# Performance work log

Hardware: AMD Instinct MI355X
Metric: run time of the kernel (lower is better)

## Reference

```python
import jax, jax.numpy as jnp
import numpy as np

N_NODES = 50000
N_EDGES = 1600000
N_FEAT = 128
EMB = 128
N_CLASSES = 10
N_GRAPHS = 512


def setup_inputs() -> dict:
    key = jax.random.key(0)
    ks = jax.random.split(key, 12)
    x = jax.random.normal(ks[0], (N_NODES, N_FEAT), dtype=jnp.float32)
    edge_index = jax.random.randint(ks[1], (2, N_EDGES), 0, N_NODES, dtype=jnp.int64)
    batch = jnp.sort(jax.random.randint(ks[2], (N_NODES,), 0, N_GRAPHS, dtype=jnp.int64))
    def glorot(k, fan_in, fan_out):
        lim = jnp.sqrt(6.0 / (fan_in + fan_out)).astype(jnp.float32)
        return jax.random.uniform(k, (fan_in, fan_out), jnp.float32, -lim, lim)
    W0 = glorot(ks[3], N_FEAT, EMB); b0 = jnp.zeros((EMB,), jnp.float32)
    W1 = glorot(ks[4], EMB, EMB);    b1 = jnp.zeros((EMB,), jnp.float32)
    W2 = glorot(ks[5], EMB, EMB);    b2 = jnp.zeros((EMB,), jnp.float32)
    Wout = glorot(ks[6], EMB, N_CLASSES)
    bout = jnp.zeros((N_CLASSES,), jnp.float32)
    return {"x": x, "edge_index": edge_index, "batch": batch,
            "W0": W0, "b0": b0, "W1": W1, "b1": b1, "W2": W2, "b2": b2,
            "Wout": Wout, "bout": bout}


def _gcn_conv(x, W, b, src, dst, norm, n_nodes):
    # PyG GCNConv: h = x @ W; aggregate norm * h[src] into dst; add bias.
    h = x @ W                                  # [N, out]
    msg = h[src] * norm[:, None]               # [E+N, out] gather (incl. self-loops)
    out = jax.ops.segment_sum(msg, dst, num_segments=n_nodes)
    return out + b


def reference(x, edge_index, batch, W0, b0, W1, b1, W2, b2, Wout, bout):
    n_nodes = x.shape[0]
    # add self-loops (GCNConv default add_self_loops=True)
    loops = jnp.arange(n_nodes, dtype=edge_index.dtype)
    src = jnp.concatenate([edge_index[0], loops])
    dst = jnp.concatenate([edge_index[1], loops])
    # symmetric normalization D^{-1/2} (A+I) D^{-1/2}
    deg = jax.ops.segment_sum(jnp.ones_like(dst, dtype=x.dtype), dst,
                              num_segments=n_nodes)
    deg_inv_sqrt = jnp.where(deg > 0, jax.lax.rsqrt(jnp.maximum(deg, 1.0)), 0.0)
    norm = deg_inv_sqrt[src] * deg_inv_sqrt[dst]   # [E+N]
    out = jnp.tanh(_gcn_conv(x, W0, b0, src, dst, norm, n_nodes))
    out = jnp.tanh(_gcn_conv(out, W1, b1, src, dst, norm, n_nodes))
    out = _gcn_conv(out, W2, b2, src, dst, norm, n_nodes)
    # global mean pool over per-node graph ids
    sums = jax.ops.segment_sum(out, batch, num_segments=N_GRAPHS)
    counts = jax.ops.segment_sum(jnp.ones((n_nodes,), out.dtype), batch,
                                 num_segments=N_GRAPHS)
    pooled = sums / jnp.maximum(counts, 1.0)[:, None]   # [G, EMB]
    logits = pooled @ Wout + bout                        # [G, C]
    return jax.nn.log_softmax(logits, axis=1)
```

## Files before the change

### kernel.cpp

```cpp
#include <hip/hip_runtime.h>
#include <math.h>


#define BLK_EDGES 4096
#define MAXB 128
#define ECAP 2048
#define WS_STRIDE 136

typedef __attribute__((ext_vector_type(8))) short bf16x8;
typedef __attribute__((ext_vector_type(4))) float f32x4;

static __device__ inline unsigned short f2bf(float f) {
    unsigned u = __float_as_uint(f);
    unsigned r = (u + 0x7FFFu + ((u >> 16) & 1u)) >> 16;
    return (unsigned short)r;
}
static __device__ inline float bf_lo(unsigned u) { return __uint_as_float(u << 16); }
static __device__ inline float bf_hi(unsigned u) { return __uint_as_float(u & 0xFFFF0000u); }
static __device__ inline unsigned char f2fp8(float v) {
    v = fminf(fmaxf(v, -240.f), 240.f);
    int u = __builtin_amdgcn_cvt_pk_fp8_f32(v, v, 0, false);
    return (unsigned char)(u & 0xFF);
}

__global__ __launch_bounds__(256) void blk_hist(const int* __restrict__ dst,
        int* __restrict__ histT, int E, int NBLK, int NB) {
    __shared__ int h[MAXB];
    int blk = blockIdx.x, t = threadIdx.x;
    for (int i = t; i < NB; i += 256) h[i] = 0;
    __syncthreads();
    int lo = blk * BLK_EDGES;
    int hi = min(E, lo + BLK_EDGES);
    for (int i = lo + t; i < hi; i += 256)
        atomicAdd(&h[dst[i] >> 9], 1);
    __syncthreads();
    for (int i = t; i < NB; i += 256) histT[i * NBLK + blk] = h[i];
}

__global__ void scan_block(const int* __restrict__ cnt, int* __restrict__ off,
                           int* __restrict__ bsum, int n) {
    __shared__ int lds[256];
    int t = threadIdx.x;
    int i = blockIdx.x * 256 + t;
    int v = (i < n) ? cnt[i] : 0;
    lds[t] = v;
    __syncthreads();
    for (int d = 1; d < 256; d <<= 1) {
        int add = (t >= d) ? lds[t - d] : 0;
        __syncthreads();
        lds[t] += add;
        __syncthreads();
    }
    if (i < n) off[i] = lds[t] - v;
    if (t == 255) bsum[blockIdx.x] = lds[255];
}

__global__ void scan_top(const int* __restrict__ bsum, int* __restrict__ boff,
                         int nblocks) {
    __shared__ int lds[256];
    int t = threadIdx.x;
    int v = (t < nblocks) ? bsum[t] : 0;
    lds[t] = v;
    __syncthreads();
    for (int d = 1; d < 256; d <<= 1) {
        int add = (t >= d) ? lds[t - d] : 0;
        __syncthreads();
        lds[t] += add;
        __syncthreads();
    }
    if (t < nblocks) boff[t] = lds[t] - v;
}

__global__ __launch_bounds__(256) void scatter_packed(const int* __restrict__ src,
        const int* __restrict__ dst, const int* __restrict__ P,
        const int* __restrict__ boff, unsigned* __restrict__ packed,
        int E, int NBLK, int NB) {
    __shared__ int cur[MAXB];
    int blk = blockIdx.x, t = threadIdx.x;
    for (int i = t; i < NB; i += 256) {
        int idx = i * NBLK + blk;
        cur[i] = P[idx] + boff[idx >> 8];
    }
    __syncthreads();
    int lo = blk * BLK_EDGES;
    int hi = min(E, lo + BLK_EDGES);
    for (int i = lo + t; i < hi; i += 256) {
        int d = dst[i];
        int pos = atomicAdd(&cur[d >> 9], 1);
        packed[pos] = ((unsigned)d << 16) | (unsigned)src[i];
    }
}

__global__ __launch_bounds__(256) void bucket_build(const unsigned* __restrict__ packed,
        const int* __restrict__ P, const int* __restrict__ boff, int* __restrict__ off,
        float* __restrict__ dis, unsigned short* __restrict__ csr16,
        int E, int NBLK, int N, int NB) {
    __shared__ int cnt[512];
    __shared__ int loc[512];
    __shared__ int ps[256];
    int b = blockIdx.x, t = threadIdx.x;
    int i0 = b * NBLK, i1 = (b + 1) * NBLK;
    int start = P[i0] + boff[i0 >> 8];
    int end   = (b == NB - 1) ? E : (P[i1] + boff[i1 >> 8]);
    cnt[t] = 0; cnt[t + 256] = 0;
    __syncthreads();
    for (int i = start + t; i < end; i += 256)
        atomicAdd(&cnt[(packed[i] >> 16) & 511], 1);
    __syncthreads();
    int c0 = cnt[2 * t], c1 = cnt[2 * t + 1];
    ps[t] = c0 + c1;
    __syncthreads();
    for (int d = 1; d < 256; d <<= 1) {
        int add = (t >= d) ? ps[t - d] : 0;
        __syncthreads();
        ps[t] += add;
        __syncthreads();
    }
    int pexcl = ps[t] - (c0 + c1);
    loc[2 * t]     = start + pexcl;
    loc[2 * t + 1] = start + pexcl + c0;
    __syncthreads();
    int node0 = b * 512;
    for (int l = t; l < 512; l += 256) {
        int node = node0 + l;
        if (node < N) {
            off[node] = loc[l];
            dis[node] = rsqrtf((float)cnt[l] + 1.0f);
        }
    }
    if (b == NB - 1 && t == 0) off[N] = E;
    __syncthreads();
    for (int i = start + t; i < end; i += 256) {
        unsigned p = packed[i];
        int l = (p >> 16) & 511;
        int pos = atomicAdd(&loc[l], 1);
        csr16[pos] = (unsigned short)(p & 0xFFFFu);
    }
}

__global__ __launch_bounds__(256) void prep(const float* __restrict__ W0,
        const float* __restrict__ W1, const float* __restrict__ W2,
        unsigned short* __restrict__ wt0, unsigned short* __restrict__ wt1,
        unsigned short* __restrict__ wt2, const float* __restrict__ x,
        unsigned short* __restrict__ xb, int n4) {
    int i = blockIdx.x * 256 + threadIdx.x;
    if (i < 3 * 16384) {
        int w = i >> 14, j = i & 16383;
        int k = j >> 7, n2 = j & 127;
        const float* Wp = (w == 0) ? W0 : (w == 1) ? W1 : W2;
        unsigned short* Wt = (w == 0) ? wt0 : (w == 1) ? wt1 : wt2;
        Wt[n2 * 128 + k] = f2bf(Wp[k * 128 + n2]);
    } else {
        int j = i - 3 * 16384;
        if (j < n4) {
            float4 f = ((const float4*)x)[j];
            ushort4 o = {f2bf(f.x), f2bf(f.y), f2bf(f.z), f2bf(f.w)};
            ((ushort4*)xb)[j] = o;
        }
    }
}

__global__ __launch_bounds__(128) void gemm_mfma(const unsigned short* __restrict__ A16,
        const unsigned short* __restrict__ Wt, const float* __restrict__ dis,
        unsigned char* __restrict__ Hs8, int n) {
    __shared__ unsigned short Ws[128 * WS_STRIDE];
    int t = threadIdx.x;
    for (int i = t; i < 128 * 16; i += 128) {
        int r = i >> 4, j = i & 15;
        uint4 u = ((const uint4*)(Wt + r * 128))[j];
        *(uint4*)&Ws[r * WS_STRIDE + j * 8] = u;
    }
    __syncthreads();

    int wave = t >> 6, lane = t & 63;
    int quad = lane >> 4, l16 = lane & 15;
    int row0 = blockIdx.x * 64 + wave * 32;

    int ra0 = row0 + l16;      if (ra0 >= n) ra0 = n - 1;
    int ra1 = row0 + 16 + l16; if (ra1 >= n) ra1 = n - 1;

    f32x4 acc[2][8];
    const f32x4 z = {0.f, 0.f, 0.f, 0.f};
#pragma unroll
    for (int mi = 0; mi < 2; ++mi)
#pragma unroll
        for (int ni = 0; ni < 8; ++ni) acc[mi][ni] = z;

#pragma unroll
    for (int ks = 0; ks < 4; ++ks) {
        int kof = ks * 32 + quad * 8;
        bf16x8 a0 = *(const bf16x8*)(A16 + (size_t)ra0 * 128 + kof);
        bf16x8 a1 = *(const bf16x8*)(A16 + (size_t)ra1 * 128 + kof);
        bf16x8 b[8];
#pragma unroll
        for (int ni = 0; ni < 8; ++ni)
            b[ni] = *(const bf16x8*)&Ws[(ni * 16 + l16) * WS_STRIDE + kof];
#pragma unroll
        for (int ni = 0; ni < 8; ++ni) {
            acc[0][ni] = __builtin_amdgcn_mfma_f32_16x16x32_bf16(a0, b[ni], acc[0][ni], 0, 0, 0);
            acc[1][ni] = __builtin_amdgcn_mfma_f32_16x16x32_bf16(a1, b[ni], acc[1][ni], 0, 0, 0);
        }
    }
#pragma unroll
    for (int mi = 0; mi < 2; ++mi) {
        int rb = row0 + mi * 16 + quad * 4;
#pragma unroll
        for (int reg = 0; reg < 4; ++reg) {
            int r = rb + reg;
            if (r < n) {
                float dv = dis[r];
#pragma unroll
                for (int ni = 0; ni < 8; ++ni)
                    Hs8[(size_t)r * 128 + ni * 16 + l16] = f2fp8(acc[mi][ni][reg] * dv);
            }
        }
    }
}

template<int DO_TANH, int OUT_BF16>
__global__ __launch_bounds__(256) void aggregate3(const unsigned char* __restrict__ hs,
    const unsigned short* __restrict__ csr, const int* __restrict__ off,
    const float* __restrict__ dis, const float* __restrict__ bias,
    void* __restrict__ outp, int n) {
    __shared__ unsigned short eidx[ECAP];
    int t = threadIdx.x;
    int node0 = blockIdx.x * 4;
    int b0 = off[node0];
    int top = node0 + 4 < n ? node0 + 4 : n;
    int b4 = off[top];
    int mblk = b4 - b0;
    bool staged = (mblk <= ECAP);
    if (staged)
        for (int i = t; i < mblk; i += 256) eidx[i] = csr[b0 + i];
    __syncthreads();

    int node = node0 + (t >> 6);
    if (node >= n) return;
    int lane = t & 63;
    int half = lane >> 5;
    int fq = lane & 31;
    const unsigned* H = (const unsigned*)hs;

    int e0 = off[node];
    int e1 = off[node + 1];
    int le0 = e0 - b0;
    int m = e1 - e0;
    float ax = 0.f, ay = 0.f, az = 0.f, aw = 0.f;

    unsigned va[8], vb[8];
    auto sumB = [&](unsigned* v) {
#pragma unroll
        for (int j = 0; j < 8; ++j) {
            ax += __builtin_amdgcn_cvt_f32_fp8(v[j], 0);
            ay += __builtin_amdgcn_cvt_f32_fp8(v[j], 1);
            az += __builtin_amdgcn_cvt_f32_fp8(v[j], 2);
            aw += __builtin_amdgcn_cvt_f32_fp8(v[j], 3);
        }
    };
    auto loadL = [&](int i, unsigned* v) {
        int s[8];
#pragma unroll
        for (int j = 0; j < 8; ++j) s[j] = eidx[le0 + i + half + 2 * j];
#pragma unroll
        for (int j = 0; j < 8; ++j) v[j] = H[(size_t)s[j] * 32 + fq];
    };
    auto loadG = [&](int i, unsigned* v) {
        int s[8];
#pragma unroll
        for (int j = 0; j < 8; ++j) s[j] = csr[e0 + i + half + 2 * j];
#pragma unroll
        for (int j = 0; j < 8; ++j) v[j] = H[(size_t)s[j] * 32 + fq];
    };

    int nfull = m & ~15;
    if (staged) {
        if (nfull) {
            int B = nfull >> 4;
            loadL(0, va);
            int k = 1;
            for (; k + 1 < B; k += 2) {
                loadL(k << 4, vb);       sumB(va);
                loadL((k + 1) << 4, va); sumB(vb);
            }
            if (k < B) { loadL(k << 4, vb); sumB(va); sumB(vb); }
            else       { sumB(va); }
        }
        for (int e = nfull + half; e < m; e += 2) {
            unsigned v = H[(size_t)eidx[le0 + e] * 32 + fq];
            ax += __builtin_amdgcn_cvt_f32_fp8(v, 0);
            ay += __builtin_amdgcn_cvt_f32_fp8(v, 1);
            az += __builtin_amdgcn_cvt_f32_fp8(v, 2);
            aw += __builtin_amdgcn_cvt_f32_fp8(v, 3);
        }
    } else {
        if (nfull) {
            int B = nfull >> 4;
            loadG(0, va);
            int k = 1;
            for (; k + 1 < B; k += 2) {
                loadG(k << 4, vb);       sumB(va);
                loadG((k + 1) << 4, va); sumB(vb);
            }
            if (k < B) { loadG(k << 4, vb); sumB(va); sumB(vb); }
            else       { sumB(va); }
        }
        for (int e = nfull + half; e < m; e += 2) {
            unsigned v = H[(size_t)csr[e0 + e] * 32 + fq];
            ax += __builtin_amdgcn_cvt_f32_fp8(v, 0);
            ay += __builtin_amdgcn_cvt_f32_fp8(v, 1);
            az += __builtin_amdgcn_cvt_f32_fp8(v, 2);
            aw += __builtin_amdgcn_cvt_f32_fp8(v, 3);
        }
    }

    ax += __shfl_xor(ax, 32, 64);
    ay += __shfl_xor(ay, 32, 64);
    az += __shfl_xor(az, 32, 64);
    aw += __shfl_xor(aw, 32, 64);

    unsigned sv = H[(size_t)node * 32 + fq];
    ax += __builtin_amdgcn_cvt_f32_fp8(sv, 0);
    ay += __builtin_amdgcn_cvt_f32_fp8(sv, 1);
    az += __builtin_amdgcn_cvt_f32_fp8(sv, 2);
    aw += __builtin_amdgcn_cvt_f32_fp8(sv, 3);

    float dn = dis[node];
    float4 bv = ((const float4*)bias)[fq];
    float ox = fmaf(dn, ax, bv.x);
    float oy = fmaf(dn, ay, bv.y);
    float oz = fmaf(dn, az, bv.z);
    float ow = fmaf(dn, aw, bv.w);
    if (DO_TANH) {
        ox = tanhf(ox); oy = tanhf(oy); oz = tanhf(oz); ow = tanhf(ow);
    }
    if (half == 0) {
        if (OUT_BF16) {
            uint2 o;
            o.x = (unsigned)f2bf(ox) | ((unsigned)f2bf(oy) << 16);
            o.y = (unsigned)f2bf(oz) | ((unsigned)f2bf(ow) << 16);
            ((uint2*)outp)[(size_t)node * 32 + fq] = o;
        } else {
            float4 o = {ox, oy, oz, ow};
            *(float4*)((float*)outp + (size_t)node * 128 + fq * 4) = o;
        }
    }
}

__global__ __launch_bounds__(256) void pool_head(const float* __restrict__ act,
    const int* __restrict__ batch, const float* __restrict__ Wout,
    const float* __restrict__ bout, float* __restrict__ out, int n, int C) {
    __shared__ float psum[4][128];
    __shared__ float l[16];
    __shared__ float stats[2];
    int g = blockIdx.x;
    int t = threadIdx.x;
    int w = t >> 6;
    int lane = t & 63;
    int lo = 0, hi = n;
    while (lo < hi) { int mid = (lo + hi) >> 1; if (batch[mid] < g) lo = mid + 1; else hi = mid; }
    int lo1 = lo, hi1 = n;
    while (lo1 < hi1) { int mid = (lo1 + hi1) >> 1; if (batch[mid] < g + 1) lo1 = mid + 1; else hi1 = mid; }
    float ax = 0.f, ay = 0.f;
    for (int i = lo + w; i < lo1; i += 4) {
        const float2 v = *(const float2*)(act + (size_t)i * 128 + lane * 2);
        ax += v.x;
        ay += v.y;
    }
    psum[w][2 * lane]     = ax;
    psum[w][2 * lane + 1] = ay;
    __syncthreads();
    if (w == 0) {
        int cnt = lo1 - lo;
        float inv = 1.0f / (float)(cnt > 0 ? cnt : 1);
        float sx = (psum[0][2 * lane] + psum[1][2 * lane])
                 + (psum[2][2 * lane] + psum[3][2 * lane]);
        float sy = (psum[0][2 * lane + 1] + psum[1][2 * lane + 1])
                 + (psum[2][2 * lane + 1] + psum[3][2 * lane + 1]);
        psum[0][2 * lane]     = sx * inv;
        psum[0][2 * lane + 1] = sy * inv;
    }
    __syncthreads();
    if (t < C) {
        float acc = bout[t];
        for (int f = 0; f < 128; ++f)
            acc = fmaf(psum[0][f], Wout[(size_t)f * C + t], acc);
        l[t] = acc;
    }
    __syncthreads();
    if (t == 0) {
        float m = -1e30f;
        for (int c = 0; c < C; ++c) m = fmaxf(m, l[c]);
        float s = 0.f;
        for (int c = 0; c < C; ++c) s += expf(l[c] - m);
        stats[0] = m;
        stats[1] = logf(s);
    }
    __syncthreads();
    if (t < C) out[(size_t)g * C + t] = l[t] - stats[0] - stats[1];
}

extern "C" void kernel_launch(void* const* d_in, const int* in_sizes, int n_in,
                              void* d_out, int out_size, void* d_ws, size_t ws_size,
                              hipStream_t stream) {
    const float* x     = (const float*)d_in[0];
    const int*   edge  = (const int*)d_in[1];
    const int*   batch = (const int*)d_in[2];
    const float* W0 = (const float*)d_in[3];
    const float* b0 = (const float*)d_in[4];
    const float* W1 = (const float*)d_in[5];
    const float* b1 = (const float*)d_in[6];
    const float* W2 = (const float*)d_in[7];
    const float* b2 = (const float*)d_in[8];
    const float* Wout = (const float*)d_in[9];
    const float* bout = (const float*)d_in[10];
    float* out = (float*)d_out;

    const int N = in_sizes[0] / 128;
    const int E = in_sizes[1] / 2;
    const int C = in_sizes[10];
    const int G = out_size / C;

    const int* src = edge;
    const int* dst = edge + E;

    const int NBLK = (E + BLK_EDGES - 1) / BLK_EDGES;
    const int NB   = (N + 511) / 512;
    const int NBQ  = NB * NBLK;

    char* p = (char*)d_ws;
    auto alloc = [&](size_t bytes) -> void* {
        void* r = (void*)p;
        p += (bytes + 255) & ~(size_t)255;
        return r;
    };
    unsigned char* hs = (unsigned char*)alloc((size_t)N * 128);
    float* act    = (float*)alloc((size_t)N * 128 * 4);
    float* dis    = (float*)alloc((size_t)N * 4);
    int*   off    = (int*)alloc((size_t)(N + 1) * 4);
    int*   P      = (int*)alloc((size_t)(NBQ + 1) * 4);
    int*   bsum   = (int*)alloc(256 * 4);
    int*   boff   = (int*)alloc(256 * 4);
    unsigned* packed = (unsigned*)alloc((size_t)E * 4);
    unsigned short* csr16 = (unsigned short*)alloc((size_t)E * 2);
    unsigned short* wt0 = (unsigned short*)alloc(128 * 128 * 2);
    unsigned short* wt1 = (unsigned short*)alloc(128 * 128 * 2);
    unsigned short* wt2 = (unsigned short*)alloc(128 * 128 * 2);

    const int sb = (NBQ + 255) / 256;

    blk_hist<<<NBLK, 256, 0, stream>>>(dst, P, E, NBLK, NB);
    scan_block<<<sb, 256, 0, stream>>>(P, P, bsum, NBQ);
    scan_top<<<1, 256, 0, stream>>>(bsum, boff, sb);
    scatter_packed<<<NBLK, 256, 0, stream>>>(src, dst, P, boff, packed, E, NBLK, NB);
    bucket_build<<<NB, 256, 0, stream>>>(packed, P, boff, off, dis, csr16, E, NBLK, N, NB);

    unsigned short* actb = (unsigned short*)act;
    const int n4 = N * 32;
    prep<<<(3 * 16384 + n4 + 255) / 256, 256, 0, stream>>>(W0, W1, W2, wt0, wt1, wt2,
                                                           x, actb, n4);

    const int gb = (N + 63) / 64;
    const int ab = (N + 3) / 4;

    gemm_mfma<<<gb, 128, 0, stream>>>(actb, wt0, dis, hs, N);
    aggregate3<1, 1><<<ab, 256, 0, stream>>>(hs, csr16, off, dis, b0, act, N);
    gemm_mfma<<<gb, 128, 0, stream>>>(actb, wt1, dis, hs, N);
    aggregate3<1, 1><<<ab, 256, 0, stream>>>(hs, csr16, off, dis, b1, act, N);
    gemm_mfma<<<gb, 128, 0, stream>>>(actb, wt2, dis, hs, N);
    aggregate3<0, 0><<<ab, 256, 0, stream>>>(hs, csr16, off, dis, b2, act, N);

    pool_head<<<G, 256, 0, stream>>>(act, batch, Wout, bout, out, N, C);
}
```

Baseline: 335.7 us.

## Fuse x bf16 conversion into first GEMM and weight prep into histogram

The separate prep kernel goes away. Weight transposition now runs as extra blocks of the histogram kernel, and the first GEMM reads fp32 x directly and converts it to bf16 in registers. The last aggregation writes bf16 instead of fp32, and pool_head reads bf16, which halves that write and read traffic. This removes a kernel launch and a full pass over x, at the cost of slightly lower precision in the pooled sum.

```diff
diff --git a/kernel.cpp b/kernel.cpp
--- a/kernel.cpp
+++ b/kernel.cpp
@@ -23,10 +23,22 @@
     return (unsigned char)(u & 0xFF);
 }
 
-__global__ __launch_bounds__(256) void blk_hist(const int* __restrict__ dst,
-        int* __restrict__ histT, int E, int NBLK, int NB) {
+__global__ __launch_bounds__(256) void blk_hist_prep(const int* __restrict__ dst,
+        int* __restrict__ histT, int E, int NBLK, int NB,
+        const float* __restrict__ W0, const float* __restrict__ W1,
+        const float* __restrict__ W2, unsigned short* __restrict__ wt0,
+        unsigned short* __restrict__ wt1, unsigned short* __restrict__ wt2) {
     __shared__ int h[MAXB];
     int blk = blockIdx.x, t = threadIdx.x;
+    if (blk >= NBLK) {
+        int i = (blk - NBLK) * 256 + t;
+        int w = i >> 14, j = i & 16383;
+        int k = j >> 7, n2 = j & 127;
+        const float* Wp = (w == 0) ? W0 : (w == 1) ? W1 : W2;
+        unsigned short* Wt = (w == 0) ? wt0 : (w == 1) ? wt1 : wt2;
+        Wt[n2 * 128 + k] = f2bf(Wp[k * 128 + n2]);
+        return;
+    }
     for (int i = t; i < NB; i += 256) h[i] = 0;
     __syncthreads();
     int lo = blk * BLK_EDGES;
@@ -138,29 +150,8 @@
     }
 }
 
-__global__ __launch_bounds__(256) void prep(const float* __restrict__ W0,
-        const float* __restrict__ W1, const float* __restrict__ W2,
-        unsigned short* __restrict__ wt0, unsigned short* __restrict__ wt1,
-        unsigned short* __restrict__ wt2, const float* __restrict__ x,
-        unsigned short* __restrict__ xb, int n4) {
-    int i = blockIdx.x * 256 + threadIdx.x;
-    if (i < 3 * 16384) {
-        int w = i >> 14, j = i & 16383;
-        int k = j >> 7, n2 = j & 127;
-        const float* Wp = (w == 0) ? W0 : (w == 1) ? W1 : W2;
-        unsigned short* Wt = (w == 0) ? wt0 : (w == 1) ? wt1 : wt2;
-        Wt[n2 * 128 + k] = f2bf(Wp[k * 128 + n2]);
-    } else {
-        int j = i - 3 * 16384;
-        if (j < n4) {
-            float4 f = ((const float4*)x)[j];
-            ushort4 o = {f2bf(f.x), f2bf(f.y), f2bf(f.z), f2bf(f.w)};
-            ((ushort4*)xb)[j] = o;
-        }
-    }
-}
-
-__global__ __launch_bounds__(128) void gemm_mfma(const unsigned short* __restrict__ A16,
+template<int IN_F32>
+__global__ __launch_bounds__(128) void gemm_mfma(const void* __restrict__ Av,
         const unsigned short* __restrict__ Wt, const float* __restrict__ dis,
         unsigned char* __restrict__ Hs8, int n) {
     __shared__ unsigned short Ws[128 * WS_STRIDE];
@@ -189,8 +180,24 @@
 #pragma unroll
     for (int ks = 0; ks < 4; ++ks) {
         int kof = ks * 32 + quad * 8;
-        bf16x8 a0 = *(const bf16x8*)(A16 + (size_t)ra0 * 128 + kof);
-        bf16x8 a1 = *(const bf16x8*)(A16 + (size_t)ra1 * 128 + kof);
+        bf16x8 a0, a1;
+        if (IN_F32) {
+            const float* A0 = (const float*)Av + (size_t)ra0 * 128 + kof;
+            const float* A1 = (const float*)Av + (size_t)ra1 * 128 + kof;
+            float4 p0 = ((const float4*)A0)[0], p1 = ((const float4*)A0)[1];
+            float4 q0 = ((const float4*)A1)[0], q1 = ((const float4*)A1)[1];
+            a0[0] = (short)f2bf(p0.x); a0[1] = (short)f2bf(p0.y);
+            a0[2] = (short)f2bf(p0.z); a0[3] = (short)f2bf(p0.w);
+            a0[4] = (short)f2bf(p1.x); a0[5] = (short)f2bf(p1.y);
+            a0[6] = (short)f2bf(p1.z); a0[7] = (short)f2bf(p1.w);
+            a1[0] = (short)f2bf(q0.x); a1[1] = (short)f2bf(q0.y);
+            a1[2] = (short)f2bf(q0.z); a1[3] = (short)f2bf(q0.w);
+            a1[4] = (short)f2bf(q1.x); a1[5] = (short)f2bf(q1.y);
+            a1[6] = (short)f2bf(q1.z); a1[7] = (short)f2bf(q1.w);
+        } else {
+            a0 = *(const bf16x8*)((const unsigned short*)Av + (size_t)ra0 * 128 + kof);
+            a1 = *(const bf16x8*)((const unsigned short*)Av + (size_t)ra1 * 128 + kof);
+        }
         bf16x8 b[8];
 #pragma unroll
         for (int ni = 0; ni < 8; ++ni)
@@ -217,11 +224,11 @@
     }
 }
 
-template<int DO_TANH, int OUT_BF16>
+template<int DO_TANH>
 __global__ __launch_bounds__(256) void aggregate3(const unsigned char* __restrict__ hs,
     const unsigned short* __restrict__ csr, const int* __restrict__ off,
     const float* __restrict__ dis, const float* __restrict__ bias,
-    void* __restrict__ outp, int n) {
+    unsigned* __restrict__ outp, int n) {
     __shared__ unsigned short eidx[ECAP];
     int t = threadIdx.x;
     int node0 = blockIdx.x * 4;
@@ -334,19 +341,14 @@
         ox = tanhf(ox); oy = tanhf(oy); oz = tanhf(oz); ow = tanhf(ow);
     }
     if (half == 0) {
-        if (OUT_BF16) {
-            uint2 o;
-            o.x = (unsigned)f2bf(ox) | ((unsigned)f2bf(oy) << 16);
-            o.y = (unsigned)f2bf(oz) | ((unsigned)f2bf(ow) << 16);
-            ((uint2*)outp)[(size_t)node * 32 + fq] = o;
-        } else {
-            float4 o = {ox, oy, oz, ow};
-            *(float4*)((float*)outp + (size_t)node * 128 + fq * 4) = o;
-        }
-    }
-}
-
-__global__ __launch_bounds__(256) void pool_head(const float* __restrict__ act,
+        uint2 o;
+        o.x = (unsigned)f2bf(ox) | ((unsigned)f2bf(oy) << 16);
+        o.y = (unsigned)f2bf(oz) | ((unsigned)f2bf(ow) << 16);
+        *(uint2*)(outp + (size_t)node * 64 + fq * 2) = o;
+    }
+}
+
+__global__ __launch_bounds__(256) void pool_head(const unsigned* __restrict__ actb,
     const int* __restrict__ batch, const float* __restrict__ Wout,
     const float* __restrict__ bout, float* __restrict__ out, int n, int C) {
     __shared__ float psum[4][128];
@@ -362,9 +364,9 @@
     while (lo1 < hi1) { int mid = (lo1 + hi1) >> 1; if (batch[mid] < g + 1) lo1 = mid + 1; else hi1 = mid; }
     float ax = 0.f, ay = 0.f;
     for (int i = lo + w; i < lo1; i += 4) {
-        const float2 v = *(const float2*)(act + (size_t)i * 128 + lane * 2);
-        ax += v.x;
-        ay += v.y;
+        unsigned v = actb[(size_t)i * 64 + lane];
+        ax += bf_lo(v);
+        ay += bf_hi(v);
     }
     psum[w][2 * lane]     = ax;
     psum[w][2 * lane + 1] = ay;
@@ -426,6 +428,7 @@
     const int NBLK = (E + BLK_EDGES - 1) / BLK_EDGES;
     const int NB   = (N + 511) / 512;
     const int NBQ  = NB * NBLK;
+    const int PREPB = (3 * 16384) / 256;
 
     char* p = (char*)d_ws;
     auto alloc = [&](size_t bytes) -> void* {
@@ -434,7 +437,7 @@
         return r;
     };
     unsigned char* hs = (unsigned char*)alloc((size_t)N * 128);
-    float* act    = (float*)alloc((size_t)N * 128 * 4);
+    unsigned* actb = (unsigned*)alloc((size_t)N * 128 * 2);
     float* dis    = (float*)alloc((size_t)N * 4);
     int*   off    = (int*)alloc((size_t)(N + 1) * 4);
     int*   P      = (int*)alloc((size_t)(NBQ + 1) * 4);
@@ -448,26 +451,22 @@
 
     const int sb = (NBQ + 255) / 256;
 
-    blk_hist<<<NBLK, 256, 0, stream>>>(dst, P, E, NBLK, NB);
+    blk_hist_prep<<<NBLK + PREPB, 256, 0, stream>>>(dst, P, E, NBLK, NB,
+                                                    W0, W1, W2, wt0, wt1, wt2);
     scan_block<<<sb, 256, 0, stream>>>(P, P, bsum, NBQ);
     scan_top<<<1, 256, 0, stream>>>(bsum, boff, sb);
     scatter_packed<<<NBLK, 256, 0, stream>>>(src, dst, P, boff, packed, E, NBLK, NB);
     bucket_build<<<NB, 256, 0, stream>>>(packed, P, boff, off, dis, csr16, E, NBLK, N, NB);
 
-    unsigned short* actb = (unsigned short*)act;
-    const int n4 = N * 32;
-    prep<<<(3 * 16384 + n4 + 255) / 256, 256, 0, stream>>>(W0, W1, W2, wt0, wt1, wt2,
-                                                           x, actb, n4);
-
     const int gb = (N + 63) / 64;
     const int ab = (N + 3) / 4;
 
-    gemm_mfma<<<gb, 128, 0, stream>>>(actb, wt0, dis, hs, N);
-    aggregate3<1, 1><<<ab, 256, 0, stream>>>(hs, csr16, off, dis, b0, act, N);
-    gemm_mfma<<<gb, 128, 0, stream>>>(actb, wt1, dis, hs, N);
-    aggregate3<1, 1><<<ab, 256, 0, stream>>>(hs, csr16, off, dis, b1, act, N);
-    gemm_mfma<<<gb, 128, 0, stream>>>(actb, wt2, dis, hs, N);
-    aggregate3<0, 0><<<ab, 256, 0, stream>>>(hs, csr16, off, dis, b2, act, N);
-
-    pool_head<<<G, 256, 0, stream>>>(act, batch, Wout, bout, out, N, C);
-}
+    gemm_mfma<1><<<gb, 128, 0, stream>>>(x,    wt0, dis, hs, N);
+    aggregate3<1><<<ab, 256, 0, stream>>>(hs, csr16, off, dis, b0, actb, N);
+    gemm_mfma<0><<<gb, 128, 0, stream>>>(actb, wt1, dis, hs, N);
+    aggregate3<1><<<ab, 256, 0, stream>>>(hs, csr16, off, dis, b1, actb, N);
+    gemm_mfma<0><<<gb, 128, 0, stream>>>(actb, wt2, dis, hs, N);
+    aggregate3<0><<<ab, 256, 0, stream>>>(hs, csr16, off, dis, b2, actb, N);
+
+    pool_head<<<G, 256, 0, stream>>>(actb, batch, Wout, bout, out, N, C);
+}
```

Measured after the change: 331.7 us. Within noise of the previous version (-1.2%).
